# Kernel optimization log

Measured on AMD Instinct MI355X. Metric: run time of the kernel, lower is better.

Reference implementation:

```python
import jax, jax.numpy as jnp
import numpy as np

NEG_INF = -1e9  # torch code uses masked_fill with -1e9, not -inf


def setup_inputs() -> dict:
    key = jax.random.key(0)
    ks = jax.random.split(key, 6)
    B, S, WL, D1, D2, OUT = 32, 128, 20, 300, 300, 300
    sequence = jax.random.normal(ks[0], (B, S, WL, D1), dtype=jnp.float32)
    vector = jax.random.normal(ks[1], (B, S, D2), dtype=jnp.float32)
    char_masks = jax.random.randint(ks[2], (B, S, WL), 0, 2, dtype=jnp.int32)
    W = jax.random.normal(ks[3], (OUT, D1 + D2), dtype=jnp.float32) * (1.0 / np.sqrt(D1 + D2))
    b = jax.random.normal(ks[4], (OUT,), dtype=jnp.float32) * 0.01
    v = jax.random.uniform(ks[5], (OUT,), dtype=jnp.float32, minval=-0.01, maxval=0.01)
    return {"sequence": sequence, "vector": vector, "char_masks": char_masks,
            "W": W, "b": b, "v": v}


def reference(sequence, vector, char_masks, W, b, v):
    # sequence: (B,S,WL,D1); vector: (B,S,D2); char_masks: (B,S,WL)
    D1 = sequence.shape[-1]
    # Linear on concat([sequence, vector_expanded]) == split matmul (avoids
    # materializing the (B,S,WL,D1+D2) concat):
    Ws, Wv = W[:, :D1], W[:, D1:]
    lin = (jnp.einsum('bswd,od->bswo', sequence, Ws)
           + jnp.einsum('bsd,od->bso', vector, Wv)[:, :, None, :]
           + b)                       # (B,S,WL,OUT)
    score = jnp.einsum('bswo,o->bsw', jnp.tanh(lin), v)  # (B,S,WL)
    score = jnp.where(char_masks == 0, NEG_INF, score)
    alphas = jax.nn.softmax(score, axis=2)               # over word_len
    weighted = jnp.einsum('bsw,bswd->bsd', alphas, sequence)  # (B,S,D1)
    return weighted
```

## Files before the change

kernel.cpp:

```cpp
#include <hip/hip_runtime.h>
#include <math.h>

#define NEG_INF -1000000000.0f

#define WL_  20
#define D1_  300
#define D2_  300
#define OUT_ 300
#define BS_  4096
#define PPB  4
#define NBLK (BS_ / PPB)
#define BM   80
#define KS   10
#define FR   512

typedef __attribute__((ext_vector_type(8))) short bf16x8;
typedef __attribute__((ext_vector_type(8))) short short8v;
typedef __attribute__((ext_vector_type(4))) float f32x4;
typedef __attribute__((ext_vector_type(4))) unsigned int uint4v;

__device__ short g_Bpk[KS * 20 * FR];
__device__ short g_Wvpk[KS * 20 * FR];

__device__ inline short f2bf(float f) {
    unsigned u = __float_as_uint(f);
    u += 0x7FFFu + ((u >> 16) & 1u);
    return (short)(u >> 16);
}
__device__ inline float bf2f(short s) {
    return __uint_as_float(((unsigned)(unsigned short)s) << 16);
}

__device__ inline void pack_store(short* Am, int s, int lane, float4 fa, float4 fb) {
    unsigned u0 = __float_as_uint(fa.x) + 0x8000u;
    unsigned u1 = __float_as_uint(fa.y) + 0x8000u;
    unsigned u2 = __float_as_uint(fa.z) + 0x8000u;
    unsigned u3 = __float_as_uint(fa.w) + 0x8000u;
    unsigned u4 = __float_as_uint(fb.x) + 0x8000u;
    unsigned u5 = __float_as_uint(fb.y) + 0x8000u;
    unsigned u6 = __float_as_uint(fb.z) + 0x8000u;
    unsigned u7 = __float_as_uint(fb.w) + 0x8000u;
    uint4v w;
    w.x = __builtin_amdgcn_perm(u1, u0, 0x07060302u);
    w.y = __builtin_amdgcn_perm(u3, u2, 0x07060302u);
    w.z = __builtin_amdgcn_perm(u5, u4, 0x07060302u);
    w.w = __builtin_amdgcn_perm(u7, u6, 0x07060302u);
    *(uint4v*)(Am + ((size_t)s * 64 + lane) * 8) = w;
}

#define GB (KS * 20 * 64)
#define GT2 (GB + GB)

__global__ __launch_bounds__(256) void prep_small(
    const float* __restrict__ W, const float* __restrict__ bias,
    short* Bpk, short* Wvpk)
{
    if (!Bpk) { Bpk = g_Bpk; Wvpk = g_Wvpk; }
    const int id = blockIdx.x * 256 + threadIdx.x;
    if (id >= GT2) return;
    short8v o8 = {0, 0, 0, 0, 0, 0, 0, 0};
    if (id < GB) {
        const int lane = id & 63, g = id >> 6;
        const int q = lane >> 4, l15 = lane & 15;
        const int ks = g / 20, tile = g % 20;
        const int o = tile * 16 + l15, k0 = ks * 32 + q * 8;
        if (o < OUT_) {
            #pragma unroll
            for (int e = 0; e < 8; ++e) {
                const int k = k0 + e;
                if (k < D1_) o8[e] = f2bf(W[(size_t)o * (D1_ + D2_) + k]);
            }
        }
        *(short8v*)(Bpk + (size_t)id * 8) = o8;
    } else {
        const int id4 = id - GB;
        const int lane = id4 & 63, g = id4 >> 6;
        const int q = lane >> 4, l15 = lane & 15;
        const int ks = g / 20, tile = g % 20;
        const int o = tile * 16 + l15, k0 = ks * 32 + q * 8;
        if (o < OUT_) {
            #pragma unroll
            for (int e = 0; e < 8; ++e) {
                const int k = k0 + e;
                if (k < D2_)        o8[e] = f2bf(W[(size_t)o * (D1_ + D2_) + D1_ + k]);
                else if (k == 319)  o8[e] = f2bf(bias[o]);
            }
        }
        *(short8v*)(Wvpk + (size_t)id4 * 8) = o8;
    }
}

__global__ __launch_bounds__(256, 2) void attn_fused(
    const float* __restrict__ seq,
    const float* __restrict__ vec,
    const int*   __restrict__ masks,
    const float* __restrict__ vvec,
    const short* Bpk, const short* Wvpk,
    float*       __restrict__ out)
{
    if (!Bpk) { Bpk = g_Bpk; Wvpk = g_Wvpk; }

    __shared__ short Am[5 * KS * FR];
    __shared__ float sp[4][BM];
    __shared__ float alpha_lds[BM];

    const int tid  = threadIdx.x;
    const int lane = tid & 63;
    const int wv   = tid >> 6;
    const int q    = lane >> 4;
    const int l15  = lane & 15;
    const int blk  = blockIdx.x;

    {
        const float* sbase = seq + (size_t)blk * BM * D1_;
        float4 ra[13], rb[13];
        #pragma unroll
        for (int it = 0; it < 13; ++it) {
            const int s = wv + it * 4;
            float4 fa = {0.f, 0.f, 0.f, 0.f}, fb = {0.f, 0.f, 0.f, 0.f};
            if (s < 50) {
                const int tile = s / KS, ks = s % KS;
                const int row = tile * 16 + l15;
                const int k0 = ks * 32 + q * 8;
                const float* p = sbase + (size_t)row * D1_ + k0;
                if (k0 < 296) { fa = *(const float4*)p; fb = *(const float4*)(p + 4); }
                else if (k0 == 296) { fa = *(const float4*)p; }
            }
            ra[it] = fa; rb[it] = fb;
        }
        #pragma unroll
        for (int it = 0; it < 13; ++it) {
            const int s = wv + it * 4;
            if (s < 50) pack_store(Am, s, lane, ra[it], rb[it]);
        }
    }

    float vj[5];
    #pragma unroll
    for (int j = 0; j < 5; ++j) {
        const int col = wv * 80 + j * 16 + l15;
        vj[j] = (col < OUT_) ? vvec[col] : 0.f;
    }

    f32x4 vacc[5];
    #pragma unroll
    for (int j = 0; j < 5; ++j) vacc[j] = {0.f, 0.f, 0.f, 0.f};
    {
        const short* pwb = Wvpk + (size_t)(wv * 5) * FR + lane * 8;
        const float* vp = vec + (size_t)(blk * PPB + (l15 & 3)) * D2_;
        #pragma unroll
        for (int ks = 0; ks < KS; ++ks) {
            const int k0 = ks * 32 + q * 8;
            short8v av = {0, 0, 0, 0, 0, 0, 0, 0};
            if (l15 < PPB) {
                #pragma unroll
                for (int e = 0; e < 8; ++e) {
                    const int k = k0 + e;
                    if (k < D2_)       av[e] = f2bf(vp[k]);
                    else if (k == 319) av[e] = (short)0x3F80;
                }
            }
            #pragma unroll
            for (int j = 0; j < 5; ++j) {
                const bf16x8 b = *(const bf16x8*)(pwb + j * FR);
                vacc[j] = __builtin_amdgcn_mfma_f32_16x16x32_bf16(
                    (bf16x8)av, b, vacc[j], 0, 0, 0);
            }
            pwb += 20 * FR;
        }
    }
    float vlp[4][5];
    #pragma unroll
    for (int p = 0; p < 4; ++p)
        #pragma unroll
        for (int j = 0; j < 5; ++j)
            vlp[p][j] = __shfl(vacc[j][p], l15, 64);
    __syncthreads();

    f32x4 acc[5][5];
    #pragma unroll
    for (int i = 0; i < 5; ++i)
        #pragma unroll
        for (int j = 0; j < 5; ++j) acc[i][j] = {0.f, 0.f, 0.f, 0.f};

    const short* pb[5];
    #pragma unroll
    for (int j = 0; j < 5; ++j)
        pb[j] = Bpk + (size_t)(wv * 5 + j) * FR + lane * 8;

    #pragma unroll
    for (int ks = 0; ks < KS; ++ks) {
        bf16x8 a[5], b[5];
        #pragma unroll
        for (int i = 0; i < 5; ++i)
            a[i] = *(const bf16x8*)(Am + (((size_t)i * KS + ks) * 64 + lane) * 8);
        #pragma unroll
        for (int j = 0; j < 5; ++j)
            b[j] = *(const bf16x8*)(pb[j] + (size_t)ks * 20 * FR);
        #pragma unroll
        for (int i = 0; i < 5; ++i)
            #pragma unroll
            for (int j = 0; j < 5; ++j)
                acc[i][j] = __builtin_amdgcn_mfma_f32_16x16x32_bf16(a[i], b[j], acc[i][j], 0, 0, 0);
    }

    #pragma unroll
    for (int i = 0; i < 5; ++i) {
        const int pLo = (16 * i) / 20;
        const int pHi = (16 * i + 15) / 20;
        #pragma unroll
        for (int r = 0; r < 4; ++r) {
            const int row = i * 16 + q * 4 + r;
            const bool hi = (row >= 20 * pHi);
            float s = 0.f;
            #pragma unroll
            for (int j = 0; j < 5; ++j) {
                const float vlv = (pLo == pHi) ? vlp[pLo][j]
                                               : (hi ? vlp[pHi][j] : vlp[pLo][j]);
                const float x = acc[i][j][r] + vlv;
                const float e = __expf(2.f * x);
                s += (1.f - 2.f / (e + 1.f)) * vj[j];
            }
            s += __shfl_xor(s, 1, 64);
            s += __shfl_xor(s, 2, 64);
            s += __shfl_xor(s, 4, 64);
            s += __shfl_xor(s, 8, 64);
            if (l15 == 0) sp[wv][row] = s;
        }
    }
    __syncthreads();

    if (tid < 128) {
        const int p = tid >> 5;
        const int w = tid & 31;
        float s;
        if (w < WL_) {
            const int row = p * WL_ + w;
            const float sc = sp[0][row] + sp[1][row] + sp[2][row] + sp[3][row];
            const int mk = masks[(size_t)(blk * PPB + p) * WL_ + w];
            s = (mk == 0) ? NEG_INF : sc;
        } else {
            s = -INFINITY;
        }
        float m = s;
        #pragma unroll
        for (int off = 16; off; off >>= 1)
            m = fmaxf(m, __shfl_xor(m, off, 32));
        const float e = __expf(s - m);
        float sum = e;
        #pragma unroll
        for (int off = 16; off; off >>= 1)
            sum += __shfl_xor(sum, off, 32);
        if (w < WL_) alpha_lds[p * WL_ + w] = e / sum;
    }
    __syncthreads();

    if (tid < PPB * 38) {
        const int p = tid / 38, ch = tid % 38;
        const int ks2 = ch >> 2, q2 = ch & 3;
        const int wst = ch % WL_;
        float o8[8] = {0.f, 0.f, 0.f, 0.f, 0.f, 0.f, 0.f, 0.f};
        #pragma unroll
        for (int wi = 0; wi < WL_; ++wi) {
            int w = wst + wi; if (w >= WL_) w -= WL_;
            const int row = p * WL_ + w;
            const int tl = row >> 4, l = row & 15;
            const bf16x8 s8 = *(const bf16x8*)(Am + (((size_t)tl * KS + ks2) * 64 + q2 * 16 + l) * 8);
            const float a = alpha_lds[row];
            #pragma unroll
            for (int e2 = 0; e2 < 8; ++e2) o8[e2] += a * bf2f(s8[e2]);
        }
        const int d0 = ch * 8, gp = blk * PPB + p;
        float* dst = out + (size_t)gp * OUT_ + d0;
        if (d0 + 8 <= OUT_) {
            *(float4*)dst       = {o8[0], o8[1], o8[2], o8[3]};
            *(float4*)(dst + 4) = {o8[4], o8[5], o8[6], o8[7]};
        } else {
            *(float4*)dst = {o8[0], o8[1], o8[2], o8[3]};
        }
    }
}

extern "C" void kernel_launch(void* const* d_in, const int* in_sizes, int n_in,
                              void* d_out, int out_size, void* d_ws, size_t ws_size,
                              hipStream_t stream) {
    const float* seq   = (const float*)d_in[0];
    const float* vec   = (const float*)d_in[1];
    const int*   masks = (const int*)d_in[2];
    const float* W     = (const float*)d_in[3];
    const float* b     = (const float*)d_in[4];
    const float* v     = (const float*)d_in[5];
    float* out = (float*)d_out;

    constexpr size_t SZ_B = sizeof(short) * (size_t)KS * 20 * FR;
    constexpr size_t NEED = SZ_B * 2;
    short *Bpk = nullptr, *Wvpk = nullptr;
    if (d_ws && ws_size >= NEED) {
        char* p = (char*)d_ws;
        Bpk  = (short*)p; p += SZ_B;
        Wvpk = (short*)p;
    }

    prep_small<<<(GT2 + 255) / 256, 256, 0, stream>>>(W, b, Bpk, Wvpk);
    attn_fused<<<NBLK, 256, 0, stream>>>(seq, vec, masks, v, Bpk, Wvpk, out);
}
```

Before: 211.0 us.

## Hoist vector projection into separate MFMA kernel and shrink block to two positions

The vector@Wv+bias projection moves out of the fused kernel into a new kernel that does dense 16-row MFMA tiles and writes a (4096x320) fp32 buffer. The fused kernel now handles 2 positions per block (40 rows, 3 M-tiles) instead of 4 (80 rows, 5 M-tiles). This removes the mostly-idle MFMA work where only 4 of 16 rows were valid, and reduces LDS and register use for higher occupancy. In exchange it adds an extra launch, a 5 MB global round trip, and wastes 8 of 48 rows in padding.

```diff
diff --git a/kernel.cpp b/kernel.cpp
--- a/kernel.cpp
+++ b/kernel.cpp
@@ -8,11 +8,13 @@
 #define D2_  300
 #define OUT_ 300
 #define BS_  4096
-#define PPB  4
+#define PPB  2
 #define NBLK (BS_ / PPB)
-#define BM   80
+#define BM   40
+#define MT   3
 #define KS   10
 #define FR   512
+#define SLABS (MT * KS)
 
 typedef __attribute__((ext_vector_type(8))) short bf16x8;
 typedef __attribute__((ext_vector_type(8))) short short8v;
@@ -21,6 +23,7 @@
 
 __device__ short g_Bpk[KS * 20 * FR];
 __device__ short g_Wvpk[KS * 20 * FR];
+__device__ float g_vlin[(size_t)BS_ * 320];
 
 __device__ inline short f2bf(float f) {
     unsigned u = __float_as_uint(f);
@@ -90,17 +93,74 @@
     }
 }
 
+__global__ __launch_bounds__(256) void vlin_direct(
+    const float* __restrict__ vec, const short* Wvpk, float* vlin)
+{
+    if (!Wvpk) { Wvpk = g_Wvpk; vlin = g_vlin; }
+    const int mtile = blockIdx.x;
+    const int tid  = threadIdx.x;
+    const int lane = tid & 63;
+    const int wv   = tid >> 6;
+    const int q = lane >> 4, l15 = lane & 15;
+
+    const float* vp = vec + (size_t)(mtile * 16 + l15) * D2_;
+    float4 ra[KS], rb[KS];
+    #pragma unroll
+    for (int ks = 0; ks < KS; ++ks) {
+        const int k0 = ks * 32 + q * 8;
+        float4 fa = {0.f, 0.f, 0.f, 0.f}, fb = {0.f, 0.f, 0.f, 0.f};
+        if (k0 < 296) { fa = *(const float4*)(vp + k0); fb = *(const float4*)(vp + k0 + 4); }
+        else if (k0 == 296) { fa = *(const float4*)(vp + k0); }
+        ra[ks] = fa; rb[ks] = fb;
+    }
+    bf16x8 frag[KS];
+    #pragma unroll
+    for (int ks = 0; ks < KS; ++ks) {
+        const int k0 = ks * 32 + q * 8;
+        const float f[8] = {ra[ks].x, ra[ks].y, ra[ks].z, ra[ks].w,
+                            rb[ks].x, rb[ks].y, rb[ks].z, rb[ks].w};
+        short8v av = {0, 0, 0, 0, 0, 0, 0, 0};
+        #pragma unroll
+        for (int e = 0; e < 8; ++e) {
+            const int k = k0 + e;
+            if (k < D2_)       av[e] = f2bf(f[e]);
+            else if (k == 319) av[e] = (short)0x3F80;
+        }
+        frag[ks] = (bf16x8)av;
+    }
+
+    f32x4 acc[5];
+    #pragma unroll
+    for (int j = 0; j < 5; ++j) acc[j] = {0.f, 0.f, 0.f, 0.f};
+    const short* pwb = Wvpk + (size_t)(wv * 5) * FR + lane * 8;
+    #pragma unroll
+    for (int ks = 0; ks < KS; ++ks) {
+        #pragma unroll
+        for (int j = 0; j < 5; ++j) {
+            const bf16x8 b = *(const bf16x8*)(pwb + j * FR);
+            acc[j] = __builtin_amdgcn_mfma_f32_16x16x32_bf16(frag[ks], b, acc[j], 0, 0, 0);
+        }
+        pwb += 20 * FR;
+    }
+    const int row0 = mtile * 16 + q * 4;
+    #pragma unroll
+    for (int j = 0; j < 5; ++j)
+        #pragma unroll
+        for (int r = 0; r < 4; ++r)
+            vlin[(size_t)(row0 + r) * 320 + (wv * 5 + j) * 16 + l15] = acc[j][r];
+}
+
 __global__ __launch_bounds__(256, 2) void attn_fused(
     const float* __restrict__ seq,
-    const float* __restrict__ vec,
     const int*   __restrict__ masks,
     const float* __restrict__ vvec,
-    const short* Bpk, const short* Wvpk,
+    const short* Bpk,
+    const float* vlinbuf,
     float*       __restrict__ out)
 {
-    if (!Bpk) { Bpk = g_Bpk; Wvpk = g_Wvpk; }
-
-    __shared__ short Am[5 * KS * FR];
+    if (!Bpk) { Bpk = g_Bpk; vlinbuf = g_vlin; }
+
+    __shared__ short Am[MT * KS * FR];
     __shared__ float sp[4][BM];
     __shared__ float alpha_lds[BM];
 
@@ -113,25 +173,27 @@
 
     {
         const float* sbase = seq + (size_t)blk * BM * D1_;
-        float4 ra[13], rb[13];
-        #pragma unroll
-        for (int it = 0; it < 13; ++it) {
+        float4 ra[8], rb[8];
+        #pragma unroll
+        for (int it = 0; it < 8; ++it) {
             const int s = wv + it * 4;
             float4 fa = {0.f, 0.f, 0.f, 0.f}, fb = {0.f, 0.f, 0.f, 0.f};
-            if (s < 50) {
+            if (s < SLABS) {
                 const int tile = s / KS, ks = s % KS;
                 const int row = tile * 16 + l15;
                 const int k0 = ks * 32 + q * 8;
-                const float* p = sbase + (size_t)row * D1_ + k0;
-                if (k0 < 296) { fa = *(const float4*)p; fb = *(const float4*)(p + 4); }
-                else if (k0 == 296) { fa = *(const float4*)p; }
+                if (row < BM) {
+                    const float* p = sbase + (size_t)row * D1_ + k0;
+                    if (k0 < 296) { fa = *(const float4*)p; fb = *(const float4*)(p + 4); }
+                    else if (k0 == 296) { fa = *(const float4*)p; }
+                }
             }
             ra[it] = fa; rb[it] = fb;
         }
         #pragma unroll
-        for (int it = 0; it < 13; ++it) {
+        for (int it = 0; it < 8; ++it) {
             const int s = wv + it * 4;
-            if (s < 50) pack_store(Am, s, lane, ra[it], rb[it]);
+            if (s < SLABS) pack_store(Am, s, lane, ra[it], rb[it]);
         }
     }
 
@@ -141,45 +203,17 @@
         const int col = wv * 80 + j * 16 + l15;
         vj[j] = (col < OUT_) ? vvec[col] : 0.f;
     }
-
-    f32x4 vacc[5];
-    #pragma unroll
-    for (int j = 0; j < 5; ++j) vacc[j] = {0.f, 0.f, 0.f, 0.f};
-    {
-        const short* pwb = Wvpk + (size_t)(wv * 5) * FR + lane * 8;
-        const float* vp = vec + (size_t)(blk * PPB + (l15 & 3)) * D2_;
-        #pragma unroll
-        for (int ks = 0; ks < KS; ++ks) {
-            const int k0 = ks * 32 + q * 8;
-            short8v av = {0, 0, 0, 0, 0, 0, 0, 0};
-            if (l15 < PPB) {
-                #pragma unroll
-                for (int e = 0; e < 8; ++e) {
-                    const int k = k0 + e;
-                    if (k < D2_)       av[e] = f2bf(vp[k]);
-                    else if (k == 319) av[e] = (short)0x3F80;
-                }
-            }
-            #pragma unroll
-            for (int j = 0; j < 5; ++j) {
-                const bf16x8 b = *(const bf16x8*)(pwb + j * FR);
-                vacc[j] = __builtin_amdgcn_mfma_f32_16x16x32_bf16(
-                    (bf16x8)av, b, vacc[j], 0, 0, 0);
-            }
-            pwb += 20 * FR;
-        }
-    }
-    float vlp[4][5];
-    #pragma unroll
-    for (int p = 0; p < 4; ++p)
+    float vlp[PPB][5];
+    #pragma unroll
+    for (int p = 0; p < PPB; ++p)
         #pragma unroll
         for (int j = 0; j < 5; ++j)
-            vlp[p][j] = __shfl(vacc[j][p], l15, 64);
+            vlp[p][j] = vlinbuf[(size_t)(blk * PPB + p) * 320 + wv * 80 + j * 16 + l15];
     __syncthreads();
 
-    f32x4 acc[5][5];
-    #pragma unroll
-    for (int i = 0; i < 5; ++i)
+    f32x4 acc[MT][5];
+    #pragma unroll
+    for (int i = 0; i < MT; ++i)
         #pragma unroll
         for (int j = 0; j < 5; ++j) acc[i][j] = {0.f, 0.f, 0.f, 0.f};
 
@@ -190,33 +224,32 @@
 
     #pragma unroll
     for (int ks = 0; ks < KS; ++ks) {
-        bf16x8 a[5], b[5];
-        #pragma unroll
-        for (int i = 0; i < 5; ++i)
+        bf16x8 a[MT], b[5];
+        #pragma unroll
+        for (int i = 0; i < MT; ++i)
             a[i] = *(const bf16x8*)(Am + (((size_t)i * KS + ks) * 64 + lane) * 8);
         #pragma unroll
         for (int j = 0; j < 5; ++j)
             b[j] = *(const bf16x8*)(pb[j] + (size_t)ks * 20 * FR);
         #pragma unroll
-        for (int i = 0; i < 5; ++i)
+        for (int i = 0; i < MT; ++i)
             #pragma unroll
             for (int j = 0; j < 5; ++j)
                 acc[i][j] = __builtin_amdgcn_mfma_f32_16x16x32_bf16(a[i], b[j], acc[i][j], 0, 0, 0);
     }
 
     #pragma unroll
-    for (int i = 0; i < 5; ++i) {
-        const int pLo = (16 * i) / 20;
-        const int pHi = (16 * i + 15) / 20;
+    for (int i = 0; i < MT; ++i) {
         #pragma unroll
         for (int r = 0; r < 4; ++r) {
             const int row = i * 16 + q * 4 + r;
-            const bool hi = (row >= 20 * pHi);
+            const bool hi = (row >= 20);
             float s = 0.f;
             #pragma unroll
             for (int j = 0; j < 5; ++j) {
-                const float vlv = (pLo == pHi) ? vlp[pLo][j]
-                                               : (hi ? vlp[pHi][j] : vlp[pLo][j]);
+                const float vlv = (i == 0) ? vlp[0][j]
+                                : (i == 2) ? vlp[1][j]
+                                : (hi ? vlp[1][j] : vlp[0][j]);
                 const float x = acc[i][j][r] + vlv;
                 const float e = __expf(2.f * x);
                 s += (1.f - 2.f / (e + 1.f)) * vj[j];
@@ -225,12 +258,12 @@
             s += __shfl_xor(s, 2, 64);
             s += __shfl_xor(s, 4, 64);
             s += __shfl_xor(s, 8, 64);
-            if (l15 == 0) sp[wv][row] = s;
+            if (l15 == 0 && row < BM) sp[wv][row] = s;
         }
     }
     __syncthreads();
 
-    if (tid < 128) {
+    if (tid < PPB * 32) {
         const int p = tid >> 5;
         const int w = tid & 31;
         float s;
@@ -293,14 +326,18 @@
     float* out = (float*)d_out;
 
     constexpr size_t SZ_B = sizeof(short) * (size_t)KS * 20 * FR;
-    constexpr size_t NEED = SZ_B * 2;
+    constexpr size_t SZ_L = sizeof(float) * (size_t)BS_ * 320;
+    constexpr size_t NEED = SZ_B * 2 + SZ_L;
     short *Bpk = nullptr, *Wvpk = nullptr;
+    float *vlin = nullptr;
     if (d_ws && ws_size >= NEED) {
         char* p = (char*)d_ws;
         Bpk  = (short*)p; p += SZ_B;
-        Wvpk = (short*)p;
+        Wvpk = (short*)p; p += SZ_B;
+        vlin = (float*)p;
     }
 
     prep_small<<<(GT2 + 255) / 256, 256, 0, stream>>>(W, b, Bpk, Wvpk);
-    attn_fused<<<NBLK, 256, 0, stream>>>(seq, vec, masks, v, Bpk, Wvpk, out);
-}
+    vlin_direct<<<256, 256, 0, stream>>>(vec, Wvpk, vlin);
+    attn_fused<<<NBLK, 256, 0, stream>>>(seq, masks, v, Bpk, vlin, out);
+}
```

Measured after the change: 197.8 us. -6.3%, faster.
